# Kernel tuning notes

Hardware: AMD Instinct MI355X
Metric: run time of the kernel (lower is better)

The kernel has to match this reference:

```python
import jax, jax.numpy as jnp
import numpy as np

D = 128
N = 50000    # nodes in bond graph g
E = 500000   # edges in g == nodes in line graph lg
ELG = 500000 # edges in line graph lg


def _linear_params(key, d_in, d_out):
    k1, k2 = jax.random.split(key)
    s = 1.0 / np.sqrt(d_in)
    W = jax.random.uniform(k1, (d_in, d_out), jnp.float32, -s, s)
    b = jax.random.uniform(k2, (d_out,), jnp.float32, -s, s)
    return W, b


def setup_inputs() -> dict:
    key = jax.random.key(0)
    ks = jax.random.split(key, 32)
    inp = {
        'x': jax.random.normal(ks[0], (N, D), jnp.float32),
        'edge_x': jax.random.normal(ks[1], (E, D), jnp.float32),
        'lg_edge_attr': jax.random.normal(ks[2], (ELG, D), jnp.float32),
        'g_edge_index': jax.random.randint(ks[3], (2, E), 0, N),
        'lg_edge_index': jax.random.randint(ks[4], (2, ELG), 0, E),
    }
    i = 5
    for pre in ('eu', 'nu'):
        for nm in ('sg', 'dg', 'eg', 'su', 'du'):
            W, b = _linear_params(ks[i], D, D); i += 1
            inp[pre + '_W' + nm] = W
            inp[pre + '_b' + nm] = b
        inp[pre + '_gamma'] = jnp.ones((D,), jnp.float32)
        inp[pre + '_beta'] = jnp.zeros((D,), jnp.float32)
    return inp


def _layernorm(x, g, b):
    m = jnp.mean(x, -1, keepdims=True)
    v = jnp.var(x, -1, keepdims=True)
    return (x - m) * jax.lax.rsqrt(v + 1e-5) * g + b


def _egc(x, edge_index, edge_attr,
         Wsg, bsg, Wdg, bdg, Weg, beg, Wsu, bsu, Wdu, bdu, gamma, beta):
    # Edge-gated graph conv. PyG convention: x_i = x[dst], x_j = x[src],
    # aggregate messages at dst (edge_index[1]).
    src, dst = edge_index[0], edge_index[1]
    # Project once at node level, then gather (same math as gather-then-linear).
    sg = x @ Wsg + bsg          # src_gate(x_i) precomputed per node
    dg = x @ Wdg + bdg          # dst_gate(x_j)
    du = x @ Wdu + bdu          # dst_update(x_j)
    gate = jax.nn.silu(sg[dst] + dg[src] + edge_attr @ Weg + beg)  # [E, D]
    msg = gate * du[src]                                           # [E, D]
    aggr = jax.ops.segment_sum(msg, dst, num_segments=x.shape[0])  # [N, D]
    out = jax.nn.silu(_layernorm(x @ Wsu + bsu + aggr, gamma, beta))
    return out + x  # residual (in_channels == out_channels here)


def reference(x, edge_x, lg_edge_attr,
              eu_Wsg, eu_bsg, eu_Wdg, eu_bdg, eu_Weg, eu_beg,
              eu_Wsu, eu_bsu, eu_Wdu, eu_bdu, eu_gamma, eu_beta,
              nu_Wsg, nu_bsg, nu_Wdg, nu_bdg, nu_Weg, nu_beg,
              nu_Wsu, nu_bsu, nu_Wdu, nu_bdu, nu_gamma, nu_beta,
              g_edge_index, lg_edge_index):
    # 1) edge update on line graph (lg nodes are g's edges)
    ea = _egc(edge_x, lg_edge_index, lg_edge_attr,
              eu_Wsg, eu_bsg, eu_Wdg, eu_bdg, eu_Weg, eu_beg,
              eu_Wsu, eu_bsu, eu_Wdu, eu_bdu, eu_gamma, eu_beta)
    # 2) node update on bond graph using updated edge features
    xn = _egc(x, g_edge_index, ea,
              nu_Wsg, nu_bsg, nu_Wdg, nu_bdg, nu_Weg, nu_beg,
              nu_Wsu, nu_bsu, nu_Wdu, nu_bdu, nu_gamma, nu_beta)
    return (xn, ea)
```

## Files before the change

### kernel.cpp

```cpp
#include <hip/hip_runtime.h>
#include <stdint.h>

#define DD 128

typedef __bf16 bf16x8 __attribute__((ext_vector_type(8)));
typedef float f32x4 __attribute__((ext_vector_type(4)));
typedef unsigned short u16;
typedef u16 u16x8 __attribute__((ext_vector_type(8)));

__device__ __forceinline__ u16 f2bf(float f) {
  union { __bf16 h; u16 u; } v; v.h = (__bf16)f; return v.u;
}
__device__ __forceinline__ float bf2f(u16 b) {
  union { uint32_t u; float f; } v; v.u = (uint32_t)b << 16; return v.f;
}
__device__ __forceinline__ float silu_f(float x) {
  return x / (1.0f + __expf(-x));
}
__device__ __forceinline__ uint32_t pkbf(float lo, float hi) {
  return (uint32_t)f2bf(lo) | ((uint32_t)f2bf(hi) << 16);
}

struct ARegs { f32x4 v[8][2]; };

__device__ __forceinline__ void issue_A(ARegs& r, const float* __restrict__ src,
                                        int base, int M, int tid) {
#pragma unroll
  for (int i = 0; i < 8; ++i) {
    int id = tid + (i << 8);
    int row = id >> 4;
    int cc = id & 15;
    if (base + row < M) {
      const f32x4* p = (const f32x4*)(src + (size_t)(base + row) * DD + cc * 8);
      r.v[i][0] = __builtin_nontemporal_load(p);
      r.v[i][1] = __builtin_nontemporal_load(p + 1);
    } else {
      r.v[i][0] = (f32x4){0.f, 0.f, 0.f, 0.f};
      r.v[i][1] = (f32x4){0.f, 0.f, 0.f, 0.f};
    }
  }
}

__device__ __forceinline__ void write_A(u16* Ab, const ARegs& r, int tid) {
#pragma unroll
  for (int i = 0; i < 8; ++i) {
    int id = tid + (i << 8);
    int row = id >> 4;
    int cc = id & 15;
    u16x8 o;
    o[0] = f2bf(r.v[i][0][0]); o[1] = f2bf(r.v[i][0][1]);
    o[2] = f2bf(r.v[i][0][2]); o[3] = f2bf(r.v[i][0][3]);
    o[4] = f2bf(r.v[i][1][0]); o[5] = f2bf(r.v[i][1][1]);
    o[6] = f2bf(r.v[i][1][2]); o[7] = f2bf(r.v[i][1][3]);
    *(u16x8*)&Ab[row * DD + ((cc ^ (row & 7)) << 3)] = o;
  }
}

struct BRegs { bf16x8 b[4][4]; };

__device__ __forceinline__ void load_B(BRegs& br, const u16* __restrict__ wt,
                                       int lane, int wc) {
  int g = lane >> 4, r15 = lane & 15;
  const u16* wbase = wt + (size_t)(wc * 64 + r15) * DD;
#pragma unroll
  for (int kk = 0; kk < 4; ++kk) {
    int ko = ((kk << 2) | g) << 3;
#pragma unroll
    for (int n = 0; n < 4; ++n)
      br.b[kk][n] = *(const bf16x8*)&wbase[n * 16 * DD + ko];
  }
}

__device__ __forceinline__ void mma_stage(const u16* Ab, const BRegs& br,
                                          f32x4 acc[4][4], int lane, int wr) {
  int g = lane >> 4, r15 = lane & 15, s = r15 & 7;
#pragma unroll
  for (int kk = 0; kk < 4; ++kk) {
    bf16x8 af[4];
#pragma unroll
    for (int m = 0; m < 4; ++m) {
      int rr = wr * 64 + m * 16 + r15;
      af[m] = *(const bf16x8*)&Ab[rr * DD + ((((kk << 2) | g) ^ s) << 3)];
    }
#pragma unroll
    for (int m = 0; m < 4; ++m)
#pragma unroll
      for (int n = 0; n < 4; ++n)
        acc[m][n] = __builtin_amdgcn_mfma_f32_16x16x32_bf16(af[m], br.b[kk][n], acc[m][n], 0, 0, 0);
  }
}

__device__ __forceinline__ void init_acc(f32x4 a[4][4], const float* __restrict__ bias,
                                         int lane, int wc) {
  int l15 = lane & 15;
#pragma unroll
  for (int n = 0; n < 4; ++n) {
    float b = bias ? bias[wc * 64 + n * 16 + l15] : 0.f;
    f32x4 v = {b, b, b, b};
#pragma unroll
    for (int m = 0; m < 4; ++m) a[m][n] = v;
  }
}

__device__ __forceinline__ void store_acc(const f32x4 acc[4][4], u16* __restrict__ out,
                                          size_t rs, int co, int base, int M,
                                          int lane, int wr, int wc) {
  int l15 = lane & 15;
  bool oddl = lane & 1;
#pragma unroll
  for (int m = 0; m < 4; ++m) {
    int rb = wr * 64 + m * 16 + ((lane >> 4) << 2);
#pragma unroll
    for (int j = 0; j < 4; ++j) {
      int row = rb + j;
      bool act = (base + row < M);
      size_t rowoff = (size_t)(base + row) * rs + co;
#pragma unroll
      for (int n0 = 0; n0 < 4; n0 += 2) {
        int c0 = wc * 64 + n0 * 16 + l15;
        float v0 = acc[m][n0][j];
        float v1 = acc[m][n0 + 1][j];
        float t0 = __shfl_xor(v0, 1);
        float t1 = __shfl_xor(v1, 1);
        uint32_t pk = oddl ? pkbf(t1, v1) : pkbf(v0, t0);
        int col2 = oddl ? (c0 + 15) : c0;
        if (act) *(uint32_t*)&out[rowoff + col2] = pk;
      }
    }
  }
}

template <bool FOUR>
__global__ void __launch_bounds__(256, 2) proj_kernel(
    int M, const float* __restrict__ src, const u16* __restrict__ wt,
    const float* __restrict__ bF,
    u16* __restrict__ o_sg, u16* __restrict__ o_dgdu, u16* __restrict__ o_su) {
  __shared__ u16 Ab[128 * DD];
  int tid = threadIdx.x, lane = tid & 63, wid = tid >> 6;
  int wr = wid >> 1, wc = wid & 1;
  int base = blockIdx.x * 128;
  BRegs b0, b1;
  {
    ARegs ar;
    issue_A(ar, src, base, M, tid);
    load_B(b0, wt + 0 * 16384, lane, wc);
    write_A(Ab, ar, tid);
  }
  __syncthreads();
  f32x4 acc[4][4];
  init_acc(acc, FOUR ? bF : nullptr, lane, wc);
  mma_stage(Ab, b0, acc, lane, wr);
  if (FOUR) {
    load_B(b1, wt + 1 * 16384, lane, wc);
    store_acc(acc, o_sg, DD, 0, base, M, lane, wr, wc);
    init_acc(acc, nullptr, lane, wc);
    mma_stage(Ab, b1, acc, lane, wr);
    load_B(b0, wt + 3 * 16384, lane, wc);
    store_acc(acc, o_dgdu, 2 * DD, 0, base, M, lane, wr, wc);
    init_acc(acc, bF + 128, lane, wc);
    mma_stage(Ab, b0, acc, lane, wr);
    load_B(b1, wt + 4 * 16384, lane, wc);
    store_acc(acc, o_dgdu, 2 * DD, DD, base, M, lane, wr, wc);
    init_acc(acc, bF + 256, lane, wc);
    mma_stage(Ab, b1, acc, lane, wr);
    store_acc(acc, o_su, DD, 0, base, M, lane, wr, wc);
  } else {
    store_acc(acc, o_sg, DD, 0, base, M, lane, wr, wc);
  }
}

__global__ void __launch_bounds__(256) hist_kernel(const int* __restrict__ dst,
                                                   int Me, int* __restrict__ cnt) {
  int i = blockIdx.x * blockDim.x + threadIdx.x;
  if (i < Me) atomicAdd(&cnt[dst[i]], 1);
}

__global__ void __launch_bounds__(256) scan1_kernel(const int* __restrict__ cnt, int M,
                                                    int* __restrict__ out,
                                                    int* __restrict__ bsum) {
  __shared__ int sh[256];
  int t = threadIdx.x;
  int i0 = blockIdx.x * 1024 + t * 4;
  int v[4];
#pragma unroll
  for (int k = 0; k < 4; ++k) v[k] = (i0 + k < M) ? cnt[i0 + k] : 0;
  int s = v[0] + v[1] + v[2] + v[3];
  sh[t] = s;
  __syncthreads();
#pragma unroll
  for (int off = 1; off < 256; off <<= 1) {
    int x = (t >= off) ? sh[t - off] : 0;
    __syncthreads();
    sh[t] += x;
    __syncthreads();
  }
  int run = sh[t] - s;
  if (t == 255) bsum[blockIdx.x] = sh[255];
#pragma unroll
  for (int k = 0; k < 4; ++k) {
    if (i0 + k < M) out[i0 + k] = run;
    run += v[k];
  }
}

__global__ void __launch_bounds__(256) scan2_kernel(int* __restrict__ bsum, int NB) {
  __shared__ int sh[512];
  int t = threadIdx.x;
  for (int i = t; i < 512; i += 256) sh[i] = (i < NB) ? bsum[i] : 0;
  __syncthreads();
  for (int off = 1; off < 512; off <<= 1) {
    int tmp[2];
#pragma unroll
    for (int q = 0; q < 2; ++q) {
      int i = t + q * 256;
      tmp[q] = (i >= off) ? sh[i - off] : 0;
    }
    __syncthreads();
#pragma unroll
    for (int q = 0; q < 2; ++q) sh[t + q * 256] += tmp[q];
    __syncthreads();
  }
  for (int i = t; i < NB; i += 256) bsum[i] = (i == 0) ? 0 : sh[i - 1];
}

__global__ void __launch_bounds__(256) scan3_kernel(int* __restrict__ rowptr,
                                                    const int* __restrict__ bscan,
                                                    int M, int Medges,
                                                    int* __restrict__ head) {
  int i = blockIdx.x * blockDim.x + threadIdx.x;
  if (i < M) {
    int v = rowptr[i] + bscan[i >> 10];
    rowptr[i] = v;
    head[i] = v;
  }
  if (i == 0) rowptr[M] = Medges;
}

__global__ void __launch_bounds__(256) eid_kernel(const int* __restrict__ src,
                                                  const int* __restrict__ dst, int Me,
                                                  int* __restrict__ head,
                                                  int* __restrict__ eids,
                                                  int* __restrict__ srcs) {
  int i = blockIdx.x * blockDim.x + threadIdx.x;
  if (i < Me) {
    int s = atomicAdd(&head[dst[i]], 1);
    eids[s] = i;
    srcs[s] = src[i];
  }
}

__global__ void prep_weights(const float* __restrict__ w0, const float* __restrict__ w1,
                             const float* __restrict__ w2, const float* __restrict__ w3,
                             const float* __restrict__ w4, const float* __restrict__ w5,
                             const float* __restrict__ w6, const float* __restrict__ w7,
                             const float* __restrict__ w8, const float* __restrict__ w9,
                             u16* __restrict__ wt) {
  const float* W;
  switch (blockIdx.x) {
    case 0: W = w0; break; case 1: W = w1; break; case 2: W = w2; break;
    case 3: W = w3; break; case 4: W = w4; break; case 5: W = w5; break;
    case 6: W = w6; break; case 7: W = w7; break; case 8: W = w8; break;
    default: W = w9; break;
  }
  u16* dst = wt + blockIdx.x * 16384;
  for (int o = threadIdx.x; o < 16384; o += 256) {
    int n = o >> 7, k = o & 127;
    dst[o] = f2bf(W[k * DD + n]);
  }
}

__global__ void fold_bias(const float* __restrict__ e_sg, const float* __restrict__ e_dg,
                          const float* __restrict__ e_eg, const float* __restrict__ e_du,
                          const float* __restrict__ e_su,
                          const float* __restrict__ n_sg, const float* __restrict__ n_dg,
                          const float* __restrict__ n_eg, const float* __restrict__ n_du,
                          const float* __restrict__ n_su, float* __restrict__ out) {
  int i = threadIdx.x;
  if (i < 128) {
    out[i]        = e_sg[i] + e_dg[i] + e_eg[i];
    out[128 + i]  = e_du[i];
    out[256 + i]  = e_su[i];
    out[384 + i]  = n_sg[i] + n_dg[i] + n_eg[i];
    out[512 + i]  = n_du[i];
    out[640 + i]  = n_su[i];
  }
}

__global__ void __launch_bounds__(256) gfin_kernel(
    int M, const int* __restrict__ rptr, const int* __restrict__ eids,
    const int* __restrict__ srcs,
    const u16* __restrict__ sg_t, const u16* __restrict__ dgdu_t,
    const u16* __restrict__ su_t, const u16* __restrict__ egp,
    const float* __restrict__ gamma, const float* __restrict__ beta,
    const float* __restrict__ resid, float* __restrict__ out) {
  int gtid = blockIdx.x * blockDim.x + threadIdx.x;
  int r = gtid >> 4;
  int l16 = gtid & 15;
  if (r >= M) return;
  int c = l16 * 8;

  u16x8 sgp = *(const u16x8*)&sg_t[(size_t)r * DD + c];
  float sg[8], ax[8];
#pragma unroll
  for (int k = 0; k < 8; ++k) { sg[k] = bf2f(sgp[k]); ax[k] = 0.f; }

  int segb = rptr[r], sege = rptr[r + 1];
  for (int s = segb; s < sege; ++s) {
    int e = eids[s];
    int sv = srcs[s];
    u16x8 gp = *(const u16x8*)&egp[(size_t)e * DD + c];
    u16x8 dgp = *(const u16x8*)&dgdu_t[(size_t)sv * (2 * DD) + c];
    u16x8 dup = *(const u16x8*)&dgdu_t[(size_t)sv * (2 * DD) + DD + c];
#pragma unroll
    for (int k = 0; k < 8; ++k) {
      float g = silu_f(sg[k] + bf2f(dgp[k]) + bf2f(gp[k]));
      ax[k] += g * bf2f(dup[k]);
    }
  }

  u16x8 sup = *(const u16x8*)&su_t[(size_t)r * DD + c];
  float v[8];
  float sum = 0.f;
#pragma unroll
  for (int k = 0; k < 8; ++k) { v[k] = bf2f(sup[k]) + ax[k]; sum += v[k]; }
#pragma unroll
  for (int off = 1; off <= 8; off <<= 1) sum += __shfl_xor(sum, off);
  float mean = sum * (1.0f / 128.0f);
  float sq = 0.f;
#pragma unroll
  for (int k = 0; k < 8; ++k) { v[k] -= mean; sq += v[k] * v[k]; }
#pragma unroll
  for (int off = 1; off <= 8; off <<= 1) sq += __shfl_xor(sq, off);
  float rs = rsqrtf(sq * (1.0f / 128.0f) + 1e-5f);

  float4 gm0 = *(const float4*)&gamma[c];
  float4 gm1 = *(const float4*)&gamma[c + 4];
  float4 bt0 = *(const float4*)&beta[c];
  float4 bt1 = *(const float4*)&beta[c + 4];
  float4 rr0 = *(const float4*)&resid[(size_t)r * DD + c];
  float4 rr1 = *(const float4*)&resid[(size_t)r * DD + c + 4];
  float gmv[8] = {gm0.x, gm0.y, gm0.z, gm0.w, gm1.x, gm1.y, gm1.z, gm1.w};
  float btv[8] = {bt0.x, bt0.y, bt0.z, bt0.w, bt1.x, bt1.y, bt1.z, bt1.w};
  float rrv[8] = {rr0.x, rr0.y, rr0.z, rr0.w, rr1.x, rr1.y, rr1.z, rr1.w};
  float o[8];
#pragma unroll
  for (int k = 0; k < 8; ++k)
    o[k] = silu_f(v[k] * rs * gmv[k] + btv[k]) + rrv[k];
  float4 o0 = {o[0], o[1], o[2], o[3]};
  float4 o1 = {o[4], o[5], o[6], o[7]};
  *(float4*)&out[(size_t)r * DD + c] = o0;
  *(float4*)&out[(size_t)r * DD + c + 4] = o1;
}

extern "C" void kernel_launch(void* const* d_in, const int* in_sizes, int n_in,
                              void* d_out, int out_size, void* d_ws, size_t ws_size,
                              hipStream_t stream) {
  const float* x   = (const float*)d_in[0];
  const float* ex  = (const float*)d_in[1];
  const float* lga = (const float*)d_in[2];
  const int* gei   = (const int*)d_in[3];
  const int* lgei  = (const int*)d_in[4];
  int N   = in_sizes[0] / DD;
  int E   = in_sizes[3] / 2;
  int ELG = in_sizes[4] / 2;

  char* p = (char*)d_ws;
  size_t off = 0;
  auto alloc = [&](size_t bytes) { char* q = p + off; off += (bytes + 255) & ~255ull; return q; };

  u16* wt     = (u16*)alloc((size_t)10 * 16384 * 2);
  float* biasF = (float*)alloc(768 * 4);
  u16* sgE    = (u16*)alloc((size_t)E * DD * 2);
  u16* dgduE  = (u16*)alloc((size_t)E * 2 * DD * 2);
  u16* suE    = (u16*)alloc((size_t)E * DD * 2);
  int  maxME  = (ELG > E) ? ELG : E;
  u16* egpB   = (u16*)alloc((size_t)maxME * DD * 2);
  u16* sgN    = (u16*)alloc((size_t)N * DD * 2);
  u16* dgduN  = (u16*)alloc((size_t)N * 2 * DD * 2);
  u16* suN    = (u16*)alloc((size_t)N * DD * 2);
  int* cnt_e  = (int*)alloc((size_t)E * 4);
  int* rptr_e = (int*)alloc((size_t)(E + 1) * 4);
  int* head_e = (int*)alloc((size_t)E * 4);
  int* eids_e = (int*)alloc((size_t)ELG * 4);
  int* srcs_e = (int*)alloc((size_t)ELG * 4);
  int* cnt_n  = (int*)alloc((size_t)N * 4);
  int* rptr_n = (int*)alloc((size_t)(N + 1) * 4);
  int* head_n = (int*)alloc((size_t)N * 4);
  int* eids_n = (int*)alloc((size_t)E * 4);
  int* srcs_n = (int*)alloc((size_t)E * 4);
  int* bsum   = (int*)alloc(512 * 4);
  if (ws_size < off) return;

  float* xn_out = (float*)d_out;
  float* ea_out = (float*)d_out + (size_t)N * DD;

  prep_weights<<<10, 256, 0, stream>>>(
      (const float*)d_in[5], (const float*)d_in[7], (const float*)d_in[9],
      (const float*)d_in[13], (const float*)d_in[11],
      (const float*)d_in[17], (const float*)d_in[19], (const float*)d_in[21],
      (const float*)d_in[25], (const float*)d_in[23], wt);
  fold_bias<<<1, 128, 0, stream>>>(
      (const float*)d_in[6], (const float*)d_in[8], (const float*)d_in[10],
      (const float*)d_in[14], (const float*)d_in[12],
      (const float*)d_in[18], (const float*)d_in[20], (const float*)d_in[22],
      (const float*)d_in[26], (const float*)d_in[24], biasF);

  hipMemsetAsync(cnt_e, 0, (size_t)E * 4, stream);
  hipMemsetAsync(cnt_n, 0, (size_t)N * 4, stream);
  hist_kernel<<<(ELG + 255) / 256, 256, 0, stream>>>(lgei + ELG, ELG, cnt_e);
  hist_kernel<<<(E + 255) / 256, 256, 0, stream>>>(gei + E, E, cnt_n);

  int NBe = (E + 1023) / 1024;
  scan1_kernel<<<NBe, 256, 0, stream>>>(cnt_e, E, rptr_e, bsum);
  scan2_kernel<<<1, 256, 0, stream>>>(bsum, NBe);
  scan3_kernel<<<(E + 255) / 256, 256, 0, stream>>>(rptr_e, bsum, E, ELG, head_e);
  eid_kernel<<<(ELG + 255) / 256, 256, 0, stream>>>(lgei, lgei + ELG, ELG, head_e,
                                                    eids_e, srcs_e);

  int NBn = (N + 1023) / 1024;
  scan1_kernel<<<NBn, 256, 0, stream>>>(cnt_n, N, rptr_n, bsum);
  scan2_kernel<<<1, 256, 0, stream>>>(bsum, NBn);
  scan3_kernel<<<(N + 255) / 256, 256, 0, stream>>>(rptr_n, bsum, N, E, head_n);
  eid_kernel<<<(E + 255) / 256, 256, 0, stream>>>(gei, gei + E, E, head_n,
                                                  eids_n, srcs_n);

  proj_kernel<true><<<(E + 127) / 128, 256, 0, stream>>>(
      E, ex, wt, biasF, sgE, dgduE, suE);
  proj_kernel<false><<<(ELG + 127) / 128, 256, 0, stream>>>(
      ELG, lga, wt + 2 * 16384, nullptr, egpB, nullptr, nullptr);
  gfin_kernel<<<(E + 15) / 16, 256, 0, stream>>>(
      E, rptr_e, eids_e, srcs_e, sgE, dgduE, suE, egpB,
      (const float*)d_in[15], (const float*)d_in[16], ex, ea_out);

  proj_kernel<true><<<(N + 127) / 128, 256, 0, stream>>>(
      N, x, wt + 5 * 16384, biasF + 384, sgN, dgduN, suN);
  proj_kernel<false><<<(E + 127) / 128, 256, 0, stream>>>(
      E, ea_out, wt + 7 * 16384, nullptr, egpB, nullptr, nullptr);
  gfin_kernel<<<(N + 15) / 16, 256, 0, stream>>>(
      N, rptr_n, eids_n, srcs_n, sgN, dgduN, suN, egpB,
      (const float*)d_in[27], (const float*)d_in[28], x, xn_out);
}
```

Before: 950.6 us.

## Scatter edge projections into CSR order so aggregation reads them contiguously

The edge-attribute projection kernel now writes each output row to its CSR slot (through a per-edge position array made by the eid kernel) instead of in original edge order. The aggregation kernel can then read the projected edge features sequentially by slot index, with no eids indirection and no random gather. The cost is moved to scattered row writes in the projection kernel. Nontemporal loads on the A input are also replaced with plain loads.

```diff
diff --git a/kernel.cpp b/kernel.cpp
--- a/kernel.cpp
+++ b/kernel.cpp
@@ -32,8 +32,8 @@
     int cc = id & 15;
     if (base + row < M) {
       const f32x4* p = (const f32x4*)(src + (size_t)(base + row) * DD + cc * 8);
-      r.v[i][0] = __builtin_nontemporal_load(p);
-      r.v[i][1] = __builtin_nontemporal_load(p + 1);
+      r.v[i][0] = p[0];
+      r.v[i][1] = p[1];
     } else {
       r.v[i][0] = (f32x4){0.f, 0.f, 0.f, 0.f};
       r.v[i][1] = (f32x4){0.f, 0.f, 0.f, 0.f};
@@ -104,7 +104,8 @@
 
 __device__ __forceinline__ void store_acc(const f32x4 acc[4][4], u16* __restrict__ out,
                                           size_t rs, int co, int base, int M,
-                                          int lane, int wr, int wc) {
+                                          int lane, int wr, int wc,
+                                          const int* sPerm) {
   int l15 = lane & 15;
   bool oddl = lane & 1;
 #pragma unroll
@@ -114,7 +115,8 @@
     for (int j = 0; j < 4; ++j) {
       int row = rb + j;
       bool act = (base + row < M);
-      size_t rowoff = (size_t)(base + row) * rs + co;
+      int orow = sPerm ? (act ? sPerm[row] : 0) : (base + row);
+      size_t rowoff = (size_t)orow * rs + co;
 #pragma unroll
       for (int n0 = 0; n0 < 4; n0 += 2) {
         int c0 = wc * 64 + n0 * 16 + l15;
@@ -134,8 +136,10 @@
 __global__ void __launch_bounds__(256, 2) proj_kernel(
     int M, const float* __restrict__ src, const u16* __restrict__ wt,
     const float* __restrict__ bF,
+    const int* __restrict__ perm,
     u16* __restrict__ o_sg, u16* __restrict__ o_dgdu, u16* __restrict__ o_su) {
   __shared__ u16 Ab[128 * DD];
+  __shared__ int sPerm[128];
   int tid = threadIdx.x, lane = tid & 63, wid = tid >> 6;
   int wr = wid >> 1, wc = wid & 1;
   int base = blockIdx.x * 128;
@@ -143,6 +147,8 @@
   {
     ARegs ar;
     issue_A(ar, src, base, M, tid);
+    if (perm && tid < 128)
+      sPerm[tid] = (base + tid < M) ? perm[base + tid] : 0;
     load_B(b0, wt + 0 * 16384, lane, wc);
     write_A(Ab, ar, tid);
   }
@@ -152,20 +158,20 @@
   mma_stage(Ab, b0, acc, lane, wr);
   if (FOUR) {
     load_B(b1, wt + 1 * 16384, lane, wc);
-    store_acc(acc, o_sg, DD, 0, base, M, lane, wr, wc);
+    store_acc(acc, o_sg, DD, 0, base, M, lane, wr, wc, nullptr);
     init_acc(acc, nullptr, lane, wc);
     mma_stage(Ab, b1, acc, lane, wr);
     load_B(b0, wt + 3 * 16384, lane, wc);
-    store_acc(acc, o_dgdu, 2 * DD, 0, base, M, lane, wr, wc);
+    store_acc(acc, o_dgdu, 2 * DD, 0, base, M, lane, wr, wc, nullptr);
     init_acc(acc, bF + 128, lane, wc);
     mma_stage(Ab, b0, acc, lane, wr);
     load_B(b1, wt + 4 * 16384, lane, wc);
-    store_acc(acc, o_dgdu, 2 * DD, DD, base, M, lane, wr, wc);
+    store_acc(acc, o_dgdu, 2 * DD, DD, base, M, lane, wr, wc, nullptr);
     init_acc(acc, bF + 256, lane, wc);
     mma_stage(Ab, b1, acc, lane, wr);
-    store_acc(acc, o_su, DD, 0, base, M, lane, wr, wc);
+    store_acc(acc, o_su, DD, 0, base, M, lane, wr, wc, nullptr);
   } else {
-    store_acc(acc, o_sg, DD, 0, base, M, lane, wr, wc);
+    store_acc(acc, o_sg, DD, 0, base, M, lane, wr, wc, perm ? sPerm : nullptr);
   }
 }
 
@@ -239,13 +245,13 @@
 __global__ void __launch_bounds__(256) eid_kernel(const int* __restrict__ src,
                                                   const int* __restrict__ dst, int Me,
                                                   int* __restrict__ head,
-                                                  int* __restrict__ eids,
-                                                  int* __restrict__ srcs) {
+                                                  int* __restrict__ srcs,
+                                                  int* __restrict__ pos) {
   int i = blockIdx.x * blockDim.x + threadIdx.x;
   if (i < Me) {
     int s = atomicAdd(&head[dst[i]], 1);
-    eids[s] = i;
     srcs[s] = src[i];
+    pos[i] = s;
   }
 }
 
@@ -287,7 +293,7 @@
 }
 
 __global__ void __launch_bounds__(256) gfin_kernel(
-    int M, const int* __restrict__ rptr, const int* __restrict__ eids,
+    int M, const int* __restrict__ rptr,
     const int* __restrict__ srcs,
     const u16* __restrict__ sg_t, const u16* __restrict__ dgdu_t,
     const u16* __restrict__ su_t, const u16* __restrict__ egp,
@@ -306,9 +312,8 @@
 
   int segb = rptr[r], sege = rptr[r + 1];
   for (int s = segb; s < sege; ++s) {
-    int e = eids[s];
     int sv = srcs[s];
-    u16x8 gp = *(const u16x8*)&egp[(size_t)e * DD + c];
+    u16x8 gp = *(const u16x8*)&egp[(size_t)s * DD + c];
     u16x8 dgp = *(const u16x8*)&dgdu_t[(size_t)sv * (2 * DD) + c];
     u16x8 dup = *(const u16x8*)&dgdu_t[(size_t)sv * (2 * DD) + DD + c];
 #pragma unroll
@@ -381,13 +386,13 @@
   int* cnt_e  = (int*)alloc((size_t)E * 4);
   int* rptr_e = (int*)alloc((size_t)(E + 1) * 4);
   int* head_e = (int*)alloc((size_t)E * 4);
-  int* eids_e = (int*)alloc((size_t)ELG * 4);
   int* srcs_e = (int*)alloc((size_t)ELG * 4);
+  int* pos_e  = (int*)alloc((size_t)ELG * 4);
   int* cnt_n  = (int*)alloc((size_t)N * 4);
   int* rptr_n = (int*)alloc((size_t)(N + 1) * 4);
   int* head_n = (int*)alloc((size_t)N * 4);
-  int* eids_n = (int*)alloc((size_t)E * 4);
   int* srcs_n = (int*)alloc((size_t)E * 4);
+  int* pos_n  = (int*)alloc((size_t)E * 4);
   int* bsum   = (int*)alloc(512 * 4);
   if (ws_size < off) return;
 
@@ -415,28 +420,28 @@
   scan2_kernel<<<1, 256, 0, stream>>>(bsum, NBe);
   scan3_kernel<<<(E + 255) / 256, 256, 0, stream>>>(rptr_e, bsum, E, ELG, head_e);
   eid_kernel<<<(ELG + 255) / 256, 256, 0, stream>>>(lgei, lgei + ELG, ELG, head_e,
-                                                    eids_e, srcs_e);
+                                                    srcs_e, pos_e);
 
   int NBn = (N + 1023) / 1024;
   scan1_kernel<<<NBn, 256, 0, stream>>>(cnt_n, N, rptr_n, bsum);
   scan2_kernel<<<1, 256, 0, stream>>>(bsum, NBn);
   scan3_kernel<<<(N + 255) / 256, 256, 0, stream>>>(rptr_n, bsum, N, E, head_n);
   eid_kernel<<<(E + 255) / 256, 256, 0, stream>>>(gei, gei + E, E, head_n,
-                                                  eids_n, srcs_n);
+                                                  srcs_n, pos_n);
 
   proj_kernel<true><<<(E + 127) / 128, 256, 0, stream>>>(
-      E, ex, wt, biasF, sgE, dgduE, suE);
+      E, ex, wt, biasF, nullptr, sgE, dgduE, suE);
   proj_kernel<false><<<(ELG + 127) / 128, 256, 0, stream>>>(
-      ELG, lga, wt + 2 * 16384, nullptr, egpB, nullptr, nullptr);
+      ELG, lga, wt + 2 * 16384, nullptr, pos_e, egpB, nullptr, nullptr);
   gfin_kernel<<<(E + 15) / 16, 256, 0, stream>>>(
-      E, rptr_e, eids_e, srcs_e, sgE, dgduE, suE, egpB,
+      E, rptr_e, srcs_e, sgE, dgduE, suE, egpB,
       (const float*)d_in[15], (const float*)d_in[16], ex, ea_out);
 
   proj_kernel<true><<<(N + 127) / 128, 256, 0, stream>>>(
-      N, x, wt + 5 * 16384, biasF + 384, sgN, dgduN, suN);
+      N, x, wt + 5 * 16384, biasF + 384, nullptr, sgN, dgduN, suN);
   proj_kernel<false><<<(E + 127) / 128, 256, 0, stream>>>(
-      E, ea_out, wt + 7 * 16384, nullptr, egpB, nullptr, nullptr);
+      E, ea_out, wt + 7 * 16384, nullptr, pos_n, egpB, nullptr, nullptr);
   gfin_kernel<<<(N + 15) / 16, 256, 0, stream>>>(
-      N, rptr_n, eids_n, srcs_n, sgN, dgduN, suN, egpB,
+      N, rptr_n, srcs_n, sgN, dgduN, suN, egpB,
       (const float*)d_in[27], (const float*)d_in[28], x, xn_out);
 }
```

New measurement: 916.4 us. -3.6%, faster.
